# Optimization experiments

Hardware: AMD Instinct MI355X
Metric: run time of the kernel (lower is better)

The kernel has to match this reference:

```python
import jax, jax.numpy as jnp
import numpy as np

B, S, C, D, V = 64, 128, 32, 512, 20000

def setup_inputs() -> dict:
    key = jax.random.key(0)
    ks = jax.random.split(key, 16)
    sc = 1.0 / np.sqrt(D)
    emb = jax.random.normal(ks[0], (V + 1, D), jnp.float32) * 0.02
    emb = emb.at[V].set(0.0)  # padding_idx=-1 -> last row zero
    inp = dict(
        emb=emb,
        W_all_w=jax.random.uniform(ks[1], (4 * D, D), jnp.float32, -sc, sc),
        W_all_b=jnp.zeros((4 * D,), jnp.float32),
        U_all_w=jax.random.uniform(ks[2], (4 * D, D), jnp.float32, -sc, sc),
        U_all_b=jnp.zeros((4 * D,), jnp.float32),
        W_d_w=jax.random.uniform(ks[3], (D, D), jnp.float32, -sc, sc),
        W_d_b=jnp.zeros((D,), jnp.float32),
        sel_w=jax.random.uniform(ks[4], (64, 1), jnp.float32, -1.0, 1.0),
        sel_b=jnp.zeros((64,), jnp.float32),
        time_w=jax.random.uniform(ks[5], (D, 64), jnp.float32, -0.125, 0.125),
        time_b=jnp.zeros((D,), jnp.float32),
        out_w=jax.random.uniform(ks[6], (2, D), jnp.float32, -sc, sc),
        out_b=jnp.zeros((2,), jnp.float32),
        seq_time_step=jax.random.uniform(ks[7], (B, S), jnp.float32, 0.0, 365.0),
        input_seqs=jax.random.randint(ks[8], (B, S, C), 0, V),
        mask=jnp.zeros((B, S), bool),
        lengths=jax.random.randint(ks[9], (B,), 1, S),
        codemask=jnp.zeros((B, S, C), bool),
        label=jax.random.randint(ks[10], (B,), 0, 2),
    )
    return inp


def reference(emb, W_all_w, W_all_b, U_all_w, U_all_b, W_d_w, W_d_b,
              sel_w, sel_b, time_w, time_b, out_w, out_b, seq_time_step,
              input_seqs, mask, lengths, codemask, label):
    # visit embedding: sum code embeddings -> [B,S,D]
    x = emb[input_seqs].sum(axis=2)
    # time feature: 1 - tanh(selection_layer(t/180)^2) -> time_layer -> [B,S,D]
    t = (seq_time_step / 180.0)[..., None]                      # [B,S,1]
    tf = 1.0 - jnp.tanh(jnp.square(t * sel_w[:, 0] + sel_b))    # [B,S,64]
    tf = jnp.einsum('bsk,dk->bsd', tf, time_w) + time_b         # [B,S,D]
    # precompute input projection for all steps: [B,S,4D]
    ux = jnp.einsum('bsd,ed->bse', x, U_all_w) + U_all_b

    def step(carry, inputs):
        h, c = carry
        tf_s, ux_s = inputs                                      # [B,D], [B,4D]
        c_s1 = jnp.tanh(c @ W_d_w.T + W_d_b)
        c_adj = c - c_s1 + c_s1 * tf_s
        outs = h @ W_all_w.T + W_all_b + ux_s
        f, i, o, c_tmp = jnp.split(jax.nn.sigmoid(outs), 4, axis=1)
        c_new = f * c_adj + i * c_tmp
        h_new = o * jnp.tanh(c_new)
        return (h_new, c_new), h_new

    h0 = jnp.zeros((B, D), x.dtype)
    c0 = jnp.zeros((B, D), x.dtype)
    tf_t = jnp.swapaxes(tf, 0, 1)   # [S,B,D]
    ux_t = jnp.swapaxes(ux, 0, 1)   # [S,B,4D]
    _, hs = jax.lax.scan(step, (h0, c0), (tf_t, ux_t))
    outputs = jnp.swapaxes(hs, 0, 1)           # [B,S,D]
    pooled = outputs.max(axis=1)                # MaxPoolLayer without mask
    out = pooled @ out_w.T + out_b              # [B,2]
    return out
```

## Files before the change

kernel.cpp:

```cpp
#include <hip/hip_runtime.h>
#include <hip/hip_bf16.h>

#define B_ 64
#define S_ 128
#define C_ 32
#define D_ 512
#define V_ 20000

typedef float     f32x4  __attribute__((ext_vector_type(4)));
typedef _Float16  f16x8  __attribute__((ext_vector_type(8)));

#define AS1 __attribute__((address_space(1)))
#define AS3 __attribute__((address_space(3)))

#define OFF_XH   0ull
#define OFF_UH   8388608ull
#define OFF_AW   10485760ull
#define OFF_CB   13631488ull
#define OFF_PAD  13639680ull
#define OFF_TWT  13647872ull
#define OFF_EMBH 13778944ull
#define OFF_TF   34259968ull
#define OFF_UX   42648576ull
#define OFF_XB2  76203008ull

#define SENT32 0x7FFF7FFFu

__global__ void k_prep_fused(
    const float* __restrict__ outb, float* __restrict__ outv,
    int4* __restrict__ fillp,
    const float* __restrict__ Wallb, const float* __restrict__ Uallb,
    float* __restrict__ cb,
    const float* __restrict__ tw, float* __restrict__ twt,
    const float* __restrict__ U, _Float16* __restrict__ uh,
    const float* __restrict__ Wall, const float* __restrict__ Wd,
    int4* __restrict__ AW,
    const float* __restrict__ emb, _Float16* __restrict__ eh)
{
    const int blk = blockIdx.x;
    const int t   = threadIdx.x;
    if (blk < 1) {
        if (t < 128) outv[t] = outb[t & 1];
    } else if (blk < 4097) {
        fillp[(blk - 1) * 256 + t] =
            int4{(int)SENT32, (int)SENT32, (int)SENT32, (int)SENT32};
    } else if (blk < 4098) {
        #pragma unroll
        for (int k = 0; k < 8; k++) {
            int i = t * 8 + k;
            cb[i] = Wallb[i] + Uallb[i];
        }
    } else if (blk < 4130) {
        int i2 = (blk - 4098) * 256 + t;
        #pragma unroll
        for (int k = 0; k < 4; k++) {
            int i = i2 * 4 + k;
            twt[(i & 63) * 512 + (i >> 6)] = tw[i];
        }
    } else if (blk < 5154) {
        int i = (blk - 4130) * 256 + t;
        float4 v = ((const float4*)U)[i];
        union { _Float16 h[4]; unsigned long long u; } pk;
        pk.h[0] = (_Float16)v.x; pk.h[1] = (_Float16)v.y;
        pk.h[2] = (_Float16)v.z; pk.h[3] = (_Float16)v.w;
        ((unsigned long long*)uh)[i] = pk.u;
    } else if (blk < 5922) {
        int i = (blk - 5154) * 256 + t;
        int lane = i & 63;  int r = i >> 6;
        int kt = r & 15;    r >>= 4;
        int tile = r % 3;   r /= 3;
        int w = r & 7;      int m = r >> 3;
        int row16 = lane & 15, quad = lane >> 4;
        int q = tile * 2 + (row16 >> 3);
        int d = m * 64 + w * 8 + (row16 & 7);
        int k0 = kt * 32 + quad * 8;
        union { _Float16 h[8]; int4 v; } u;
        const float* src = nullptr;
        if (q < 4)       src = Wall + (size_t)(q * 512 + d) * 512 + k0;
        else if (q == 4) src = Wd   + (size_t)d * 512 + k0;
        #pragma unroll
        for (int j = 0; j < 8; j++) u.h[j] = src ? (_Float16)src[j] : (_Float16)0.f;
        AW[i] = u.v;
    } else {
        int i = (blk - 5922) * 256 + t;
        float2 v = ((const float2*)emb)[i];
        unsigned short hx = __builtin_bit_cast(unsigned short, (_Float16)v.x);
        unsigned short hy = __builtin_bit_cast(unsigned short, (_Float16)v.y);
        ((unsigned*)eh)[i] = (unsigned)hx | ((unsigned)hy << 16);
    }
}

__global__ void k_embed2(const _Float16* __restrict__ embh, const int* __restrict__ seqs,
                         _Float16* __restrict__ xh)
{
    int bs = blockIdx.x;
    int t  = threadIdx.x;
    __shared__ int rows[32];
    if (t < 32) {
        int r = seqs[(size_t)bs * C_ + t];
        rows[t] = (r < 0) ? V_ : r;
    }
    __syncthreads();
    float ax = 0.f, ay = 0.f;
    #pragma unroll 4
    for (int c = 0; c < C_; c++) {
        unsigned v = *(const unsigned*)(embh + (size_t)rows[c] * D_ + 2 * t);
        ax += (float)__builtin_bit_cast(_Float16, (unsigned short)v);
        ay += (float)__builtin_bit_cast(_Float16, (unsigned short)(v >> 16));
    }
    unsigned short hx = __builtin_bit_cast(unsigned short, (_Float16)ax);
    unsigned short hy = __builtin_bit_cast(unsigned short, (_Float16)ay);
    *(unsigned*)(xh + (size_t)bs * D_ + 2 * t) = (unsigned)hx | ((unsigned)hy << 16);
}

__global__ __launch_bounds__(512) void k_tf2(
    const float* __restrict__ stime, const float* __restrict__ selw,
    const float* __restrict__ selb, const float* __restrict__ twT,
    const float* __restrict__ timeb, _Float16* __restrict__ tf)
{
    int bb = blockIdx.x;
    int t  = threadIdx.x;
    __shared__ float s1[16][64];
    for (int idx = t; idx < 1024; idx += 512) {
        int bl = idx >> 6, j = idx & 63;
        float tv = stime[bb * 16 + bl] * (1.0f / 180.0f);
        float u  = tv * selw[j] + selb[j];
        s1[bl][j] = 1.0f - tanhf(u * u);
    }
    __syncthreads();
    int d = t;
    float acc[16];
    float tb = timeb[d];
    #pragma unroll
    for (int l = 0; l < 16; l++) acc[l] = tb;
    for (int j = 0; j < 64; j++) {
        float wj = twT[j * 512 + d];
        #pragma unroll
        for (int l = 0; l < 16; l++) acc[l] = fmaf(s1[l][j], wj, acc[l]);
    }
    #pragma unroll
    for (int l = 0; l < 16; l++)
        tf[(size_t)(bb * 16 + l) * 512 + d] = (_Float16)acc[l];
}

__device__ __forceinline__ void stage16(const _Float16* g, _Float16* l)
{
#if __has_builtin(__builtin_amdgcn_global_load_lds)
    __builtin_amdgcn_global_load_lds((const AS1 void*)g, (AS3 void*)l, 16, 0, 0);
#else
    *(int4*)l = *(const int4*)g;
#endif
}

__global__ __launch_bounds__(256, 4) void k_gemm3(const _Float16* __restrict__ A,
                                                  const _Float16* __restrict__ Bm,
                                                  _Float16* __restrict__ Cg)
{
    __shared__ __align__(16) _Float16 As[128 * 64];
    __shared__ __align__(16) _Float16 Bs[128 * 64];
    const int t = threadIdx.x;
    const int w = t >> 6, lane = t & 63;
    const int wm = w & 1, wn = w >> 1;
    const int m0 = blockIdx.y * 128, n0 = blockIdx.x * 128;
    const int r16 = lane & 15, quad = lane >> 4;

    const int srow = w * 8 + (lane >> 3);
    const int k8g  = (lane & 7) ^ ((lane >> 3) & 7);
    const _Float16* ga = A  + (size_t)(m0 + srow) * 512 + k8g * 8;
    const _Float16* gb = Bm + (size_t)(n0 + srow) * 512 + k8g * 8;
    _Float16* la = As + srow * 64 + (lane & 7) * 8;
    _Float16* lb = Bs + srow * 64 + (lane & 7) * 8;

    f32x4 acc[4][4] = {};
    for (int k0 = 0; k0 < 512; k0 += 64) {
        __syncthreads();
        #pragma unroll
        for (int r = 0; r < 4; r++) {
            stage16(ga + k0 + (size_t)r * 32 * 512, la + r * 32 * 64);
            stage16(gb + k0 + (size_t)r * 32 * 512, lb + r * 32 * 64);
        }
        __syncthreads();
        #pragma unroll
        for (int sub = 0; sub < 2; sub++) {
            f16x8 af[4], bf[4];
            const int ksl = ((sub * 4 + quad) ^ (r16 & 7)) * 8;
            #pragma unroll
            for (int i = 0; i < 4; i++) {
                af[i] = *(const f16x8*)(As + (wm * 64 + i * 16 + r16) * 64 + ksl);
                bf[i] = *(const f16x8*)(Bs + (wn * 64 + i * 16 + r16) * 64 + ksl);
            }
            #pragma unroll
            for (int i = 0; i < 4; i++)
                #pragma unroll
                for (int j = 0; j < 4; j++)
                    acc[i][j] = __builtin_amdgcn_mfma_f32_16x16x32_f16(
                                    af[i], bf[j], acc[i][j], 0, 0, 0);
        }
    }
    #pragma unroll
    for (int i = 0; i < 4; i++)
        #pragma unroll
        for (int j = 0; j < 4; j++) {
            int row = m0 + wm * 64 + i * 16 + quad * 4;
            int col = n0 + wn * 64 + j * 16 + r16;
            _Float16* cp = Cg + (size_t)row * 2048 + col;
            #pragma unroll
            for (int rg = 0; rg < 4; rg++)
                cp[(size_t)rg * 2048] = (_Float16)acc[i][j][rg];
        }
}

__device__ __forceinline__ float fsigm(float x)
{
    return __builtin_amdgcn_rcpf(1.f + __expf(-x));
}
__device__ __forceinline__ float ftanh(float x)
{
    return 1.f - 2.f * __builtin_amdgcn_rcpf(1.f + __expf(2.f * x));
}

__global__ __launch_bounds__(512, 2) void k_rnn7x(
    const int4* __restrict__ AW,
    const float* __restrict__ cbv, const float* __restrict__ wdb,
    const _Float16* __restrict__ ux, const _Float16* __restrict__ tf,
    const float* __restrict__ outw,
    float* __restrict__ out,
    unsigned long long* __restrict__ xb64)
{
    const int t    = threadIdx.x;
    const int xcd  = blockIdx.x & 7;
    const int jj   = blockIdx.x >> 3;
    const int gid  = xcd * 4 + (jj & 3);
    const int m    = jj >> 2;
    const int b0   = gid * 2;
    const int w    = t >> 6;
    const int lane = t & 63;
    const int col  = lane & 15;
    const int quad = lane >> 4;

    int4 Af[48];
    {
        const int4* src = AW + (size_t)(m * 8 + w) * 3072;
        #pragma unroll
        for (int i = 0; i < 48; i++) Af[i] = src[i * 64 + lane];
    }

    __shared__ __align__(16) _Float16 xstg[4 * 544];
    __shared__ __align__(16) float cmat[8][4][48];
    __shared__ float pstg[2][64];

    const bool act = (lane < 16);
    const int  pb  = lane >> 3;
    const int  pj  = lane & 7;
    const int  dl  = w * 8 + pj;
    const int  d   = m * 64 + dl;

    float cbf = 0, cbi = 0, cbo = 0, cbc = 0, bdv = 0;
    if (act) {
        cbf = cbv[d]; cbi = cbv[512 + d]; cbo = cbv[1024 + d]; cbc = cbv[1536 + d];
        bdv = wdb[d];
    }
    float c_reg = 0.f, pool = -1e30f;
    const int dw = w * 64 + lane;

    for (int s = 0; s < S_; s++) {
        float uf = 0, ui = 0, uo = 0, uc = 0, tv = 0;
        if (act) {
            size_t bs = (size_t)(b0 + pb) * S_ + s;
            const _Float16* up = ux + bs * 2048 + d;
            uf = (float)up[0];    ui = (float)up[512];
            uo = (float)up[1024]; uc = (float)up[1536];
            tv = (float)tf[bs * 512 + d];
        }

        unsigned long long val = 0ull;
        if (s > 0) {
            const unsigned long long* src =
                xb64 + (((size_t)s * 32 + gid) * 8 + w) * 64 + lane;
            int tries = 0;
            for (;;) {
                val = __hip_atomic_load(src, __ATOMIC_RELAXED,
                                        __HIP_MEMORY_SCOPE_AGENT);
                if ((unsigned)val != SENT32 && (unsigned)(val >> 32) != SENT32)
                    break;
                if (++tries > (1 << 22)) break;
            }
        }
        __syncthreads();
        xstg[0 * 544 + dw] = __builtin_bit_cast(_Float16, (unsigned short)(val));
        xstg[2 * 544 + dw] = __builtin_bit_cast(_Float16, (unsigned short)(val >> 16));
        xstg[1 * 544 + dw] = __builtin_bit_cast(_Float16, (unsigned short)(val >> 32));
        xstg[3 * 544 + dw] = __builtin_bit_cast(_Float16, (unsigned short)(val >> 48));
        __syncthreads();

        f32x4 a0 = {0, 0, 0, 0}, a1 = {0, 0, 0, 0}, a2 = {0, 0, 0, 0};
        #pragma unroll
        for (int kt = 0; kt < 16; kt++) {
            f16x8 b = {};
            if (col < 4)
                b = *(const f16x8*)(xstg + col * 544 + kt * 32 + quad * 8);
            a0 = __builtin_amdgcn_mfma_f32_16x16x32_f16(
                     __builtin_bit_cast(f16x8, Af[kt]),      b, a0, 0, 0, 0);
            a1 = __builtin_amdgcn_mfma_f32_16x16x32_f16(
                     __builtin_bit_cast(f16x8, Af[16 + kt]), b, a1, 0, 0, 0);
            a2 = __builtin_amdgcn_mfma_f32_16x16x32_f16(
                     __builtin_bit_cast(f16x8, Af[32 + kt]), b, a2, 0, 0, 0);
        }

        if (col < 4) {
            *(f32x4*)&cmat[w][col][ 0 + quad * 4] = a0;
            *(f32x4*)&cmat[w][col][16 + quad * 4] = a1;
            *(f32x4*)&cmat[w][col][32 + quad * 4] = a2;
        }

        if (act) {
            float f_  = cmat[w][pb][ 0 + pj];
            float i_  = cmat[w][pb][ 8 + pj];
            float o_  = cmat[w][pb][16 + pj];
            float g_  = cmat[w][pb][24 + pj];
            float wd_ = cmat[w][2 + pb][32 + pj];
            float gf = fsigm(f_ + cbf + uf);
            float gi = fsigm(i_ + cbi + ui);
            float go = fsigm(o_ + cbo + uo);
            float gc = fsigm(g_ + cbc + uc);
            float cs1  = ftanh(wd_ + bdv);
            float cadj = c_reg - cs1 + cs1 * tv;
            float cn   = gf * cadj + gi * gc;
            float hn   = go * ftanh(cn);
            c_reg = cn;
            pool  = fmaxf(pool, hn);
            unsigned hh = __builtin_bit_cast(unsigned short, (_Float16)hn);
            unsigned cc = __builtin_bit_cast(unsigned short, (_Float16)cn);
            unsigned pk = hh | (cc << 16);
            unsigned other = __shfl(pk, lane + 8);
            if (pb == 0 && s != S_ - 1) {
                unsigned long long ov =
                    (unsigned long long)pk | ((unsigned long long)other << 32);
                unsigned long long* dst =
                    xb64 + (((size_t)(s + 1) * 32 + gid) * 8 + m) * 64 + dl;
                __hip_atomic_store(dst, ov, __ATOMIC_RELAXED,
                                   __HIP_MEMORY_SCOPE_AGENT);
            }
        }
    }

    if (act) pstg[pb][dl] = pool;
    __syncthreads();
    if (t < 128) {
        int b = t >> 6, l = t & 63;
        float pv = pstg[b][l];
        int dg = m * 64 + l;
        float p0 = pv * outw[dg], p1 = pv * outw[512 + dg];
        #pragma unroll
        for (int off = 32; off > 0; off >>= 1) {
            p0 += __shfl_down(p0, off);
            p1 += __shfl_down(p1, off);
        }
        if (l == 0) {
            atomicAdd(&out[2 * (b0 + b)],     p0);
            atomicAdd(&out[2 * (b0 + b) + 1], p1);
        }
    }
}

extern "C" void kernel_launch(void* const* d_in, const int* in_sizes, int n_in,
                              void* d_out, int out_size, void* d_ws, size_t ws_size,
                              hipStream_t stream)
{
    const float* emb   = (const float*)d_in[0];
    const float* Wall  = (const float*)d_in[1];
    const float* Wallb = (const float*)d_in[2];
    const float* Uall  = (const float*)d_in[3];
    const float* Uallb = (const float*)d_in[4];
    const float* Wdw   = (const float*)d_in[5];
    const float* Wdb   = (const float*)d_in[6];
    const float* selw  = (const float*)d_in[7];
    const float* selb  = (const float*)d_in[8];
    const float* timew = (const float*)d_in[9];
    const float* timeb = (const float*)d_in[10];
    const float* outw  = (const float*)d_in[11];
    const float* outb  = (const float*)d_in[12];
    const float* stime = (const float*)d_in[13];
    const int*   seqs  = (const int*)d_in[14];
    float* out = (float*)d_out;
    char*  ws  = (char*)d_ws;

    _Float16* xh   = (_Float16*)(ws + OFF_XH);
    _Float16* uh   = (_Float16*)(ws + OFF_UH);
    int4*     aw   = (int4*)(ws + OFF_AW);
    float*    cbp  = (float*)(ws + OFF_CB);
    float*    twt  = (float*)(ws + OFF_TWT);
    _Float16* eh   = (_Float16*)(ws + OFF_EMBH);
    _Float16* tfp  = (_Float16*)(ws + OFF_TF);
    _Float16* uxp  = (_Float16*)(ws + OFF_UX);
    unsigned long long* xb = (unsigned long long*)(ws + OFF_XB2);

    k_prep_fused<<<25923, 256, 0, stream>>>(
        outb, out, (int4*)(ws + OFF_XB2),
        Wallb, Uallb, cbp,
        timew, twt,
        Uall, uh,
        Wall, Wdw, aw,
        emb, eh);
    k_embed2 <<<B_ * S_, 256, 0, stream>>>(eh, seqs, xh);
    k_tf2    <<<512,     512, 0, stream>>>(stime, selw, selb, twt, timeb, tfp);
    k_gemm3  <<<dim3(16, 64), 256, 0, stream>>>(xh, uh, uxp);
    k_rnn7x  <<<256,     512, 0, stream>>>(aw, cbp, Wdb, uxp, tfp, outw, out, xb);
}
```

Before: 483.3 us.

## Process two batch groups per RNN block, interleaving their recurrence phases

The recurrent kernel now runs on half as many blocks. Each block handles two independent batch groups and alternates a step of one with a step of the other, so one group's cross-block wait can overlap with the other group's compute. The weight fragments held in registers are reused across both groups. The spin-wait also falls back to system-scope atomic loads after 512 tries. In exchange, each block has twice the serial work per step, and fewer CUs stay busy.

```diff
diff --git a/kernel.cpp b/kernel.cpp
--- a/kernel.cpp
+++ b/kernel.cpp
@@ -219,7 +219,7 @@
     return 1.f - 2.f * __builtin_amdgcn_rcpf(1.f + __expf(2.f * x));
 }
 
-__global__ __launch_bounds__(512, 2) void k_rnn7x(
+__global__ __launch_bounds__(512, 2) void k_rnn12(
     const int4* __restrict__ AW,
     const float* __restrict__ cbv, const float* __restrict__ wdb,
     const _Float16* __restrict__ ux, const _Float16* __restrict__ tf,
@@ -230,9 +230,9 @@
     const int t    = threadIdx.x;
     const int xcd  = blockIdx.x & 7;
     const int jj   = blockIdx.x >> 3;
-    const int gid  = xcd * 4 + (jj & 3);
-    const int m    = jj >> 2;
-    const int b0   = gid * 2;
+    const int pr   = xcd * 2 + (jj & 1);
+    const int m    = jj >> 1;
+    const int gidA = pr * 2, gidB = pr * 2 + 1;
     const int w    = t >> 6;
     const int lane = t & 63;
     const int col  = lane & 15;
@@ -247,7 +247,7 @@
 
     __shared__ __align__(16) _Float16 xstg[4 * 544];
     __shared__ __align__(16) float cmat[8][4][48];
-    __shared__ float pstg[2][64];
+    __shared__ float pstg[2][2][64];
 
     const bool act = (lane < 16);
     const int  pb  = lane >> 3;
@@ -260,95 +260,107 @@
         cbf = cbv[d]; cbi = cbv[512 + d]; cbo = cbv[1024 + d]; cbc = cbv[1536 + d];
         bdv = wdb[d];
     }
-    float c_reg = 0.f, pool = -1e30f;
+    float c_regA = 0.f, poolA = -1e30f;
+    float c_regB = 0.f, poolB = -1e30f;
     const int dw = w * 64 + lane;
 
+#define RNN_PHASE(GID, CREG, POOL)                                              \
+    {                                                                           \
+        const int b0 = (GID) * 2;                                               \
+        float uf = 0, ui = 0, uo = 0, uc = 0, tv = 0;                           \
+        if (act) {                                                              \
+            size_t bs = (size_t)(b0 + pb) * S_ + s;                             \
+            const _Float16* up = ux + bs * 2048 + d;                            \
+            uf = (float)up[0];    ui = (float)up[512];                          \
+            uo = (float)up[1024]; uc = (float)up[1536];                         \
+            tv = (float)tf[bs * 512 + d];                                       \
+        }                                                                       \
+        unsigned long long val = 0ull;                                          \
+        if (s > 0) {                                                            \
+            const unsigned long long* src =                                     \
+                xb64 + (((size_t)s * 32 + (GID)) * 8 + w) * 64 + lane;          \
+            int tries = 0;                                                      \
+            for (;;) {                                                          \
+                val = (tries < 512)                                             \
+                    ? __hip_atomic_load(src, __ATOMIC_RELAXED,                  \
+                                        __HIP_MEMORY_SCOPE_AGENT)              \
+                    : __hip_atomic_load(src, __ATOMIC_RELAXED,                  \
+                                        __HIP_MEMORY_SCOPE_SYSTEM);            \
+                if ((unsigned)val != SENT32 && (unsigned)(val >> 32) != SENT32) \
+                    break;                                                      \
+                if (++tries > (1 << 22)) break;                                 \
+            }                                                                   \
+        }                                                                       \
+        __syncthreads();               \
+        xstg[0 * 544 + dw] = __builtin_bit_cast(_Float16, (unsigned short)(val)); \
+        xstg[2 * 544 + dw] = __builtin_bit_cast(_Float16, (unsigned short)(val >> 16)); \
+        xstg[1 * 544 + dw] = __builtin_bit_cast(_Float16, (unsigned short)(val >> 32)); \
+        xstg[3 * 544 + dw] = __builtin_bit_cast(_Float16, (unsigned short)(val >> 48)); \
+        __syncthreads();                               \
+        f32x4 a0 = {0, 0, 0, 0}, a1 = {0, 0, 0, 0}, a2 = {0, 0, 0, 0};          \
+        _Pragma("unroll")                                                       \
+        for (int kt = 0; kt < 16; kt++) {                                       \
+            f16x8 b = {};                                                       \
+            if (col < 4)                                                        \
+                b = *(const f16x8*)(xstg + col * 544 + kt * 32 + quad * 8);     \
+            a0 = __builtin_amdgcn_mfma_f32_16x16x32_f16(                        \
+                     __builtin_bit_cast(f16x8, Af[kt]),      b, a0, 0, 0, 0);   \
+            a1 = __builtin_amdgcn_mfma_f32_16x16x32_f16(                        \
+                     __builtin_bit_cast(f16x8, Af[16 + kt]), b, a1, 0, 0, 0);   \
+            a2 = __builtin_amdgcn_mfma_f32_16x16x32_f16(                        \
+                     __builtin_bit_cast(f16x8, Af[32 + kt]), b, a2, 0, 0, 0);   \
+        }                                                                       \
+        if (col < 4) {                                                          \
+            *(f32x4*)&cmat[w][col][ 0 + quad * 4] = a0;                         \
+            *(f32x4*)&cmat[w][col][16 + quad * 4] = a1;                         \
+            *(f32x4*)&cmat[w][col][32 + quad * 4] = a2;                         \
+        }                                                                       \
+        if (act) {                                                              \
+            float f_  = cmat[w][pb][ 0 + pj];                                   \
+            float i_  = cmat[w][pb][ 8 + pj];                                   \
+            float o_  = cmat[w][pb][16 + pj];                                   \
+            float g_  = cmat[w][pb][24 + pj];                                   \
+            float wd_ = cmat[w][2 + pb][32 + pj];                               \
+            float gf = fsigm(f_ + cbf + uf);                                    \
+            float gi = fsigm(i_ + cbi + ui);                                    \
+            float go = fsigm(o_ + cbo + uo);                                    \
+            float gc = fsigm(g_ + cbc + uc);                                    \
+            float cs1  = ftanh(wd_ + bdv);                                      \
+            float cadj = (CREG) - cs1 + cs1 * tv;                               \
+            float cn   = gf * cadj + gi * gc;                                   \
+            float hn   = go * ftanh(cn);                                        \
+            (CREG) = cn;                                                        \
+            (POOL) = fmaxf((POOL), hn);                                         \
+            unsigned hh = __builtin_bit_cast(unsigned short, (_Float16)hn);     \
+            unsigned cc = __builtin_bit_cast(unsigned short, (_Float16)cn);     \
+            unsigned pk = hh | (cc << 16);                                      \
+            unsigned other = __shfl(pk, lane + 8);                              \
+            if (pb == 0 && s != S_ - 1) {                                       \
+                unsigned long long ov =                                         \
+                    (unsigned long long)pk | ((unsigned long long)other << 32); \
+                unsigned long long* dst =                                       \
+                    xb64 + (((size_t)(s + 1) * 32 + (GID)) * 8 + m) * 64 + dl;  \
+                __hip_atomic_store(dst, ov, __ATOMIC_RELAXED,                   \
+                                   __HIP_MEMORY_SCOPE_AGENT);                  \
+            }                                                                   \
+        }                                                                       \
+    }
+
     for (int s = 0; s < S_; s++) {
-        float uf = 0, ui = 0, uo = 0, uc = 0, tv = 0;
-        if (act) {
-            size_t bs = (size_t)(b0 + pb) * S_ + s;
-            const _Float16* up = ux + bs * 2048 + d;
-            uf = (float)up[0];    ui = (float)up[512];
-            uo = (float)up[1024]; uc = (float)up[1536];
-            tv = (float)tf[bs * 512 + d];
-        }
-
-        unsigned long long val = 0ull;
-        if (s > 0) {
-            const unsigned long long* src =
-                xb64 + (((size_t)s * 32 + gid) * 8 + w) * 64 + lane;
-            int tries = 0;
-            for (;;) {
-                val = __hip_atomic_load(src, __ATOMIC_RELAXED,
-                                        __HIP_MEMORY_SCOPE_AGENT);
-                if ((unsigned)val != SENT32 && (unsigned)(val >> 32) != SENT32)
-                    break;
-                if (++tries > (1 << 22)) break;
-            }
-        }
-        __syncthreads();
-        xstg[0 * 544 + dw] = __builtin_bit_cast(_Float16, (unsigned short)(val));
-        xstg[2 * 544 + dw] = __builtin_bit_cast(_Float16, (unsigned short)(val >> 16));
-        xstg[1 * 544 + dw] = __builtin_bit_cast(_Float16, (unsigned short)(val >> 32));
-        xstg[3 * 544 + dw] = __builtin_bit_cast(_Float16, (unsigned short)(val >> 48));
-        __syncthreads();
-
-        f32x4 a0 = {0, 0, 0, 0}, a1 = {0, 0, 0, 0}, a2 = {0, 0, 0, 0};
-        #pragma unroll
-        for (int kt = 0; kt < 16; kt++) {
-            f16x8 b = {};
-            if (col < 4)
-                b = *(const f16x8*)(xstg + col * 544 + kt * 32 + quad * 8);
-            a0 = __builtin_amdgcn_mfma_f32_16x16x32_f16(
-                     __builtin_bit_cast(f16x8, Af[kt]),      b, a0, 0, 0, 0);
-            a1 = __builtin_amdgcn_mfma_f32_16x16x32_f16(
-                     __builtin_bit_cast(f16x8, Af[16 + kt]), b, a1, 0, 0, 0);
-            a2 = __builtin_amdgcn_mfma_f32_16x16x32_f16(
-                     __builtin_bit_cast(f16x8, Af[32 + kt]), b, a2, 0, 0, 0);
-        }
-
-        if (col < 4) {
-            *(f32x4*)&cmat[w][col][ 0 + quad * 4] = a0;
-            *(f32x4*)&cmat[w][col][16 + quad * 4] = a1;
-            *(f32x4*)&cmat[w][col][32 + quad * 4] = a2;
-        }
-
-        if (act) {
-            float f_  = cmat[w][pb][ 0 + pj];
-            float i_  = cmat[w][pb][ 8 + pj];
-            float o_  = cmat[w][pb][16 + pj];
-            float g_  = cmat[w][pb][24 + pj];
-            float wd_ = cmat[w][2 + pb][32 + pj];
-            float gf = fsigm(f_ + cbf + uf);
-            float gi = fsigm(i_ + cbi + ui);
-            float go = fsigm(o_ + cbo + uo);
-            float gc = fsigm(g_ + cbc + uc);
-            float cs1  = ftanh(wd_ + bdv);
-            float cadj = c_reg - cs1 + cs1 * tv;
-            float cn   = gf * cadj + gi * gc;
-            float hn   = go * ftanh(cn);
-            c_reg = cn;
-            pool  = fmaxf(pool, hn);
-            unsigned hh = __builtin_bit_cast(unsigned short, (_Float16)hn);
-            unsigned cc = __builtin_bit_cast(unsigned short, (_Float16)cn);
-            unsigned pk = hh | (cc << 16);
-            unsigned other = __shfl(pk, lane + 8);
-            if (pb == 0 && s != S_ - 1) {
-                unsigned long long ov =
-                    (unsigned long long)pk | ((unsigned long long)other << 32);
-                unsigned long long* dst =
-                    xb64 + (((size_t)(s + 1) * 32 + gid) * 8 + m) * 64 + dl;
-                __hip_atomic_store(dst, ov, __ATOMIC_RELAXED,
-                                   __HIP_MEMORY_SCOPE_AGENT);
-            }
-        }
-    }
-
-    if (act) pstg[pb][dl] = pool;
+        RNN_PHASE(gidA, c_regA, poolA)
+        RNN_PHASE(gidB, c_regB, poolB)
+    }
+#undef RNN_PHASE
+
+    if (act) {
+        pstg[0][pb][dl] = poolA;
+        pstg[1][pb][dl] = poolB;
+    }
     __syncthreads();
-    if (t < 128) {
-        int b = t >> 6, l = t & 63;
-        float pv = pstg[b][l];
+    if (t < 256) {
+        int ch = t >> 7, b = (t >> 6) & 1, l = t & 63;
+        float pv = pstg[ch][b][l];
+        int batch = (pr * 2 + ch) * 2 + b;
         int dg = m * 64 + l;
         float p0 = pv * outw[dg], p1 = pv * outw[512 + dg];
         #pragma unroll
@@ -357,8 +369,8 @@
             p1 += __shfl_down(p1, off);
         }
         if (l == 0) {
-            atomicAdd(&out[2 * (b0 + b)],     p0);
-            atomicAdd(&out[2 * (b0 + b) + 1], p1);
+            atomicAdd(&out[2 * batch],     p0);
+            atomicAdd(&out[2 * batch + 1], p1);
         }
     }
 }
@@ -405,5 +417,5 @@
     k_embed2 <<<B_ * S_, 256, 0, stream>>>(eh, seqs, xh);
     k_tf2    <<<512,     512, 0, stream>>>(stime, selw, selb, twt, timeb, tfp);
     k_gemm3  <<<dim3(16, 64), 256, 0, stream>>>(xh, uh, uxp);
-    k_rnn7x  <<<256,     512, 0, stream>>>(aw, cbp, Wdb, uxp, tfp, outw, out, xb);
-}
+    k_rnn12  <<<128,     512, 0, stream>>>(aw, cbp, Wdb, uxp, tfp, outw, out, xb);
+}
```

Result: slower. 736.3 us (+52.4%).
